# Performance work log

Measured on AMD Instinct MI355X. Metric: run time of the kernel, lower is better.

## Reference

```python
import jax, jax.numpy as jnp
import numpy as np

N_NODES = 50000
N_EDGES = 800000
IN_F = 512
H_F = 32
HEADS = 8
N_CLS = 40
NEG_SLOPE = 0.2


def gat_conv(h, W, al, ar, b, src, dst, n_heads, d_out):
    """DGL-style GATConv. h: [N, F_in]; W: [F_in, n_heads*d_out];
    al, ar: [n_heads, d_out]; b: [n_heads*d_out]. Returns [N, n_heads, d_out]."""
    n = h.shape[0]
    feat = (h @ W).reshape(n, n_heads, d_out)            # [N, H, D]
    el = jnp.sum(feat * al[None], axis=-1)               # [N, H]
    er = jnp.sum(feat * ar[None], axis=-1)               # [N, H]
    e = jax.nn.leaky_relu(el[src] + er[dst], NEG_SLOPE)  # [E, H]
    # numerically stable edge softmax per destination node
    m = jax.ops.segment_max(e, dst, num_segments=n)      # [N, H]
    m = jnp.where(jnp.isfinite(m), m, 0.0)
    ee = jnp.exp(e - m[dst])                             # [E, H]
    den = jax.ops.segment_sum(ee, dst, num_segments=n)   # [N, H]
    alpha = ee / jnp.maximum(den[dst], 1e-9)             # [E, H]
    msg = alpha[:, :, None] * feat[src]                  # [E, H, D]
    rst = jax.ops.segment_sum(msg, dst, num_segments=n)  # [N, H, D]
    return rst + b.reshape(1, n_heads, d_out)


def setup_inputs() -> dict:
    key = jax.random.key(0)
    ks = jax.random.split(key, 16)
    hid = H_F * HEADS
    s = lambda fan: 1.0 / np.sqrt(fan)
    return {
        "in_feat": jax.random.normal(ks[0], (N_NODES, IN_F), jnp.float32),
        "src": jax.random.randint(ks[1], (N_EDGES,), 0, N_NODES, jnp.int32),
        "dst": jax.random.randint(ks[2], (N_EDGES,), 0, N_NODES, jnp.int32),
        "W0": jax.random.normal(ks[3], (IN_F, hid), jnp.float32) * s(IN_F),
        "al0": jax.random.normal(ks[4], (HEADS, H_F), jnp.float32) * s(H_F),
        "ar0": jax.random.normal(ks[5], (HEADS, H_F), jnp.float32) * s(H_F),
        "b0": jnp.zeros((hid,), jnp.float32),
        "W1": jax.random.normal(ks[6], (hid, hid), jnp.float32) * s(hid),
        "al1": jax.random.normal(ks[7], (HEADS, H_F), jnp.float32) * s(H_F),
        "ar1": jax.random.normal(ks[8], (HEADS, H_F), jnp.float32) * s(H_F),
        "b1": jnp.zeros((hid,), jnp.float32),
        "W2": jax.random.normal(ks[9], (hid, N_CLS), jnp.float32) * s(hid),
        "al2": jax.random.normal(ks[10], (1, N_CLS), jnp.float32) * s(N_CLS),
        "ar2": jax.random.normal(ks[11], (1, N_CLS), jnp.float32) * s(N_CLS),
        "b2": jnp.zeros((N_CLS,), jnp.float32),
    }


def reference(in_feat, src, dst, W0, al0, ar0, b0, W1, al1, ar1, b1,
              W2, al2, ar2, b2):
    n = in_feat.shape[0]
    # layer 0 + ReLU (dropout p=0.0 is identity) + flatten heads
    h = gat_conv(in_feat, W0, al0, ar0, b0, src, dst, HEADS, H_F)
    h = jax.nn.relu(h).reshape(n, -1)
    # layer 1
    h = gat_conv(h, W1, al1, ar1, b1, src, dst, HEADS, H_F)
    h = jax.nn.relu(h).reshape(n, -1)
    # output layer, single head, no activation
    h = gat_conv(h, W2, al2, ar2, b2, src, dst, 1, N_CLS)
    return h.reshape(n, -1)
```

## Files before the change

### kernel.cpp

```cpp
#include <hip/hip_runtime.h>
#include <hip/hip_bf16.h>

#define N_NODES 50000
#define N_EDGES 800000
#define IN_F 512
#define HID 256
#define HEADS 8
#define DHEAD 32
#define N_CLS 40
#define NCLS_PAD 64

typedef __bf16 bf16x8 __attribute__((ext_vector_type(8)));
typedef float f32x4 __attribute__((ext_vector_type(4)));
typedef float f32x2 __attribute__((ext_vector_type(2)));

#define AT_AL0 0
#define AT_AR0 256
#define AT_AL1 512
#define AT_AR1 768
#define AT_AL2 1024
#define AT_AR2 1088
#define AT_B0  1152
#define AT_B1  1408
#define AT_B2  1664
#define AT_SZ  1792

__device__ __forceinline__ float ldflag(const void* p, long long i, int isbf) {
  return isbf ? __bfloat162float(((const __hip_bfloat16*)p)[i])
              : ((const float*)p)[i];
}
__device__ __forceinline__ float blo(unsigned u) { return __uint_as_float(u << 16); }
__device__ __forceinline__ float bhi(unsigned u) { return __uint_as_float(u & 0xffff0000u); }
__device__ __forceinline__ f32x2 bpair(unsigned u) {
  f32x2 r;
  r.x = __uint_as_float(u << 16);
  r.y = __uint_as_float(u & 0xffff0000u);
  return r;
}
__device__ __forceinline__ unsigned pk2(float a, float b) {
  unsigned x = __bfloat16_as_ushort(__float2bfloat16(a));
  unsigned y = __bfloat16_as_ushort(__float2bfloat16(b));
  return x | (y << 16);
}
__device__ __forceinline__ uint4 ldA8(const void* A, int isbf, size_t base) {
  if (isbf) return *(const uint4*)((const unsigned short*)A + base);
  const float* ap = (const float*)A + base;
  float4 f1 = *(const float4*)ap;
  float4 f2 = *(const float4*)(ap + 4);
  return make_uint4(pk2(f1.x, f1.y), pk2(f1.z, f1.w), pk2(f2.x, f2.y), pk2(f2.z, f2.w));
}
__device__ __forceinline__ bf16x8 as_bf(uint4 v) {
  union { uint4 u; bf16x8 b; } x; x.u = v; return x.b;
}

__global__ void k_detect_prep(const unsigned short* __restrict__ raw, int* __restrict__ flag,
                              const void* al0, const void* ar0, const void* al1, const void* ar1,
                              const void* al2, const void* ar2, const void* b0, const void* b1,
                              const void* b2, float* __restrict__ att, int* __restrict__ cursor) {
  __shared__ int cnt[256];
  int t = threadIdx.x;
  for (int i = t; i < N_NODES; i += 256) cursor[i] = 0;
  int c = 0;
  for (int i = t; i < 8192; i += 256) {
    int e = (raw[i] >> 7) & 0xFF;
    if (e >= 0x90) c++;
  }
  cnt[t] = c;
  __syncthreads();
  for (int s = 128; s; s >>= 1) {
    if (t < s) cnt[t] += cnt[t + s];
    __syncthreads();
  }
  __shared__ int sflag;
  if (t == 0) { sflag = (cnt[0] > 64) ? 0 : 1; *flag = sflag; }
  __syncthreads();
  int isbf = sflag;
  att[AT_AL0 + t] = ldflag(al0, t, isbf);
  att[AT_AR0 + t] = ldflag(ar0, t, isbf);
  att[AT_AL1 + t] = ldflag(al1, t, isbf);
  att[AT_AR1 + t] = ldflag(ar1, t, isbf);
  att[AT_B0 + t]  = ldflag(b0, t, isbf);
  att[AT_B1 + t]  = ldflag(b1, t, isbf);
  if (t < N_CLS) {
    att[AT_AL2 + t] = ldflag(al2, t, isbf);
    att[AT_AR2 + t] = ldflag(ar2, t, isbf);
    att[AT_B2 + t]  = ldflag(b2, t, isbf);
  }
}

__global__ void k_hist(const int* __restrict__ dst, int* __restrict__ cnt) {
  int e = blockIdx.x * blockDim.x + threadIdx.x;
  if (e < N_EDGES) atomicAdd(&cnt[dst[e]], 1);
}

#define SCAN_B 512
#define SCAN_NB ((N_NODES + SCAN_B - 1) / SCAN_B)

__global__ __launch_bounds__(SCAN_B) void k_scan_blocks(const int* __restrict__ deg,
                                                        int* __restrict__ excl,
                                                        int* __restrict__ partial) {
  __shared__ int buf[SCAN_B];
  int t = threadIdx.x;
  int i = blockIdx.x * SCAN_B + t;
  int v = (i < N_NODES) ? deg[i] : 0;
  buf[t] = v;
  __syncthreads();
  for (int off = 1; off < SCAN_B; off <<= 1) {
    int x = (t >= off) ? buf[t - off] : 0;
    __syncthreads();
    buf[t] += x;
    __syncthreads();
  }
  if (i < N_NODES) excl[i] = buf[t] - v;
  if (t == SCAN_B - 1) partial[blockIdx.x] = buf[t];
}

__global__ void k_scan_partials(int* __restrict__ partial, int* __restrict__ rowptr) {
  __shared__ int buf[SCAN_NB];
  int t = threadIdx.x;
  if (t < SCAN_NB) buf[t] = partial[t];
  __syncthreads();
  if (t == 0) {
    int run = 0;
    for (int b = 0; b < SCAN_NB; b++) { int v = buf[b]; buf[b] = run; run += v; }
    rowptr[N_NODES] = run;
  }
  __syncthreads();
  if (t < SCAN_NB) partial[t] = buf[t];
}

__global__ void k_scan_add(int* __restrict__ rowptr, const int* __restrict__ partial,
                           int* __restrict__ cursor) {
  int i = blockIdx.x * blockDim.x + threadIdx.x;
  if (i < N_NODES) {
    rowptr[i] += partial[i / SCAN_B];
    cursor[i] = 0;
  }
}

__global__ void k_scatter(const int* __restrict__ src, const int* __restrict__ dst,
                          const int* __restrict__ rowptr, int* __restrict__ cursor,
                          int* __restrict__ csr_src) {
  int e = blockIdx.x * blockDim.x + threadIdx.x;
  if (e < N_EDGES) {
    int d = dst[e];
    int pos = rowptr[d] + atomicAdd(&cursor[d], 1);
    csr_src[pos] = src[e];
  }
}

#define TW0 (HID * IN_F)
#define TW1 (TW0 + HID * HID)
#define TW2 (TW1 + NCLS_PAD * HID)
__global__ void k_transpose_all(const void* __restrict__ W0, const void* __restrict__ W1,
                                const void* __restrict__ W2,
                                __hip_bfloat16* __restrict__ w0t, __hip_bfloat16* __restrict__ w1t,
                                __hip_bfloat16* __restrict__ w2t, const int* __restrict__ flag) {
  int isbf = *flag;
  int i = blockIdx.x * blockDim.x + threadIdx.x;
  if (i < TW0) {
    int n = i >> 9, k = i & 511;
    w0t[i] = __float2bfloat16(ldflag(W0, (long long)k * HID + n, isbf));
  } else if (i < TW1) {
    int j = i - TW0;
    int n = j >> 8, k = j & 255;
    w1t[j] = __float2bfloat16(ldflag(W1, (long long)k * HID + n, isbf));
  } else if (i < TW2) {
    int j = i - TW1;
    int n = j >> 8, k = j & 255;
    float v = (n < N_CLS) ? ldflag(W2, (long long)k * N_CLS + n, isbf) : 0.f;
    w2t[j] = __float2bfloat16(v);
  }
}

__global__ __launch_bounds__(256) void k_gemmw(const void* __restrict__ A,
                                               const __hip_bfloat16* __restrict__ Bt,
                                               __hip_bfloat16* __restrict__ C,
                                               int M, int K, int N,
                                               const int* __restrict__ flag, int force_bf,
                                               const float* __restrict__ al,
                                               const float* __restrict__ ar,
                                               float* __restrict__ el,
                                               float* __restrict__ er, int fuse_eler) {
  const int isbf = force_bf ? 1 : *flag;
  int nblk = N >> 6;
  int wave = threadIdx.x >> 6, lane = threadIdx.x & 63;
  int tile = blockIdx.x * 4 + wave;
  int mb = tile / nblk;
  int nb = tile - mb * nblk;
  int m0 = mb * 64, n0 = nb * 64;
  if (m0 >= M) return;
  int lm = lane & 15, quad = lane >> 4;
  int koff = quad << 3;
  size_t ab[4];
  const unsigned short* bb[4];
  #pragma unroll
  for (int i = 0; i < 4; i++) {
    int ga = m0 + i * 16 + lm;
    if (ga > M - 1) ga = M - 1;
    ab[i] = (size_t)ga * K + koff;
    bb[i] = (const unsigned short*)Bt + (size_t)(n0 + i * 16 + lm) * K + koff;
  }
  f32x4 acc[4][4] = {};
  uint4 a0[4], b0[4];
  #pragma unroll
  for (int i = 0; i < 4; i++) { a0[i] = ldA8(A, isbf, ab[i]); b0[i] = *(const uint4*)bb[i]; }
  int nk = K >> 5;
  for (int t = 1; t < nk; ++t) {
    int k0 = t << 5;
    uint4 a1[4], b1[4];
    #pragma unroll
    for (int i = 0; i < 4; i++) {
      a1[i] = ldA8(A, isbf, ab[i] + k0);
      b1[i] = *(const uint4*)(bb[i] + k0);
    }
    #pragma unroll
    for (int mi = 0; mi < 4; mi++)
      #pragma unroll
      for (int ni = 0; ni < 4; ni++)
        acc[mi][ni] = __builtin_amdgcn_mfma_f32_16x16x32_bf16(as_bf(a0[mi]), as_bf(b0[ni]),
                                                              acc[mi][ni], 0, 0, 0);
    #pragma unroll
    for (int i = 0; i < 4; i++) { a0[i] = a1[i]; b0[i] = b1[i]; }
  }
  #pragma unroll
  for (int mi = 0; mi < 4; mi++)
    #pragma unroll
    for (int ni = 0; ni < 4; ni++)
      acc[mi][ni] = __builtin_amdgcn_mfma_f32_16x16x32_bf16(as_bf(a0[mi]), as_bf(b0[ni]),
                                                            acc[mi][ni], 0, 0, 0);
  #pragma unroll
  for (int mi = 0; mi < 4; mi++) {
    #pragma unroll
    for (int r2 = 0; r2 < 4; r2++) {
      int gm = m0 + mi * 16 + (quad << 2) + r2;
      if (gm < M) {
        #pragma unroll
        for (int ni = 0; ni < 4; ni++) {
          int gn = n0 + ni * 16 + lm;
          C[(size_t)gm * N + gn] = __float2bfloat16(acc[mi][ni][r2]);
        }
      }
    }
  }
  if (fuse_eler) {
    int h0 = n0 >> 5;
    float ala[4], ara[4];
    #pragma unroll
    for (int ni = 0; ni < 4; ni++) {
      int idx = (h0 + (ni >> 1)) * DHEAD + ((ni & 1) << 4) + lm;
      ala[ni] = al[idx];
      ara[ni] = ar[idx];
    }
    #pragma unroll
    for (int mi = 0; mi < 4; mi++)
      #pragma unroll
      for (int r2 = 0; r2 < 4; r2++) {
        int gm = m0 + mi * 16 + (quad << 2) + r2;
        #pragma unroll
        for (int hp = 0; hp < 2; hp++) {
          float pl = acc[mi][2 * hp][r2] * ala[2 * hp] + acc[mi][2 * hp + 1][r2] * ala[2 * hp + 1];
          float pr = acc[mi][2 * hp][r2] * ara[2 * hp] + acc[mi][2 * hp + 1][r2] * ara[2 * hp + 1];
          #pragma unroll
          for (int d = 1; d < 16; d <<= 1) {
            pl += __shfl_xor(pl, d, 16);
            pr += __shfl_xor(pr, d, 16);
          }
          if (lm == 0 && gm < M) {
            el[gm * HEADS + h0 + hp] = pl;
            er[gm * HEADS + h0 + hp] = pr;
          }
        }
      }
  }
}

__global__ void k_eler2(const __hip_bfloat16* __restrict__ feat2,
                        const float* __restrict__ al, const float* __restrict__ ar,
                        float* __restrict__ el, float* __restrict__ er) {
  int n = blockIdx.x * blockDim.x + threadIdx.x;
  if (n >= N_NODES) return;
  const __hip_bfloat16* f = feat2 + (size_t)n * NCLS_PAD;
  float sl = 0.f, sr = 0.f;
  for (int d = 0; d < N_CLS; d++) {
    float v = __bfloat162float(f[d]);
    sl += v * al[d];
    sr += v * ar[d];
  }
  el[n] = sl;
  er[n] = sr;
}

__global__ __launch_bounds__(256) void k_aggregate8(const int* __restrict__ rowptr,
                                                    const int* __restrict__ csr_src,
                                                    const uint4* __restrict__ feat_rows,
                                                    const float* __restrict__ el,
                                                    const float* __restrict__ er,
                                                    const float* __restrict__ bias,
                                                    __hip_bfloat16* __restrict__ out) {
  __shared__ float lds_acc[8][256];
  __shared__ float lds_l[8][32];
  int n = blockIdx.x;
  int t = threadIdx.x;
  int slot = t >> 5;
  int c = t & 31;
  int hh = c >> 2;
  float er_n = er[n * HEADS + hh];
  int beg = rowptr[n], end = rowptr[n + 1];
  float l = 0.f;
  f32x2 a0 = {0.f, 0.f}, a1 = {0.f, 0.f}, a2 = {0.f, 0.f}, a3 = {0.f, 0.f};
  const char* fb = (const char*)feat_rows;
  unsigned cb = (unsigned)c << 4;
  int i = beg + slot;
  for (; i + 8 < end; i += 16) {
    int s1 = csr_src[i];
    int s2 = csr_src[i + 8];
    float el1 = el[s1 * HEADS + hh];
    float el2 = el[s2 * HEADS + hh];
    uint4 f1 = *(const uint4*)(fb + (((unsigned)s1 << 9) | cb));
    uint4 f2 = *(const uint4*)(fb + (((unsigned)s2 << 9) | cb));
    float x1 = el1 + er_n, x2 = el2 + er_n;
    float e1 = x1 > 0.f ? x1 : 0.2f * x1;
    float e2 = x2 > 0.f ? x2 : 0.2f * x2;
    float p1 = __expf(fminf(e1, 60.f));
    float p2 = __expf(fminf(e2, 60.f));
    l += p1 + p2;
    a0 += bpair(f1.x) * p1; a1 += bpair(f1.y) * p1;
    a2 += bpair(f1.z) * p1; a3 += bpair(f1.w) * p1;
    a0 += bpair(f2.x) * p2; a1 += bpair(f2.y) * p2;
    a2 += bpair(f2.z) * p2; a3 += bpair(f2.w) * p2;
  }
  if (i < end) {
    int s = csr_src[i];
    float elv = el[s * HEADS + hh];
    uint4 fv = *(const uint4*)(fb + (((unsigned)s << 9) | cb));
    float x = elv + er_n;
    float e = x > 0.f ? x : 0.2f * x;
    float p = __expf(fminf(e, 60.f));
    l += p;
    a0 += bpair(fv.x) * p; a1 += bpair(fv.y) * p;
    a2 += bpair(fv.z) * p; a3 += bpair(fv.w) * p;
  }
  *(float4*)&lds_acc[slot][c * 8]     = make_float4(a0.x, a0.y, a1.x, a1.y);
  *(float4*)&lds_acc[slot][c * 8 + 4] = make_float4(a2.x, a2.y, a3.x, a3.y);
  lds_l[slot][c] = l;
  __syncthreads();
  float a = 0.f, L = 0.f;
  #pragma unroll
  for (int s2 = 0; s2 < 8; s2++) { a += lds_acc[s2][t]; L += lds_l[s2][t >> 3]; }
  float o = a / fmaxf(L, 1e-9f) + bias[t];
  o = fmaxf(o, 0.f);
  out[(size_t)n * HID + t] = __float2bfloat16(o);
}

__global__ __launch_bounds__(256) void k_aggregate1(const int* __restrict__ rowptr,
                                                    const int* __restrict__ csr_src,
                                                    const uint4* __restrict__ fr2,
                                                    const float* __restrict__ el,
                                                    const float* __restrict__ er,
                                                    const float* __restrict__ bias,
                                                    void* __restrict__ out,
                                                    const int* __restrict__ flag) {
  __shared__ float lds_acc[32][64];
  __shared__ float lds_l[32][8];
  int isbf = *flag;
  int n = blockIdx.x;
  int t = threadIdx.x;
  int slot = t >> 3;
  int c = t & 7;
  float er_n = er[n];
  int beg = rowptr[n], end = rowptr[n + 1];
  float l = 0.f;
  f32x2 a0 = {0.f, 0.f}, a1 = {0.f, 0.f}, a2 = {0.f, 0.f}, a3 = {0.f, 0.f};
  const char* fb = (const char*)fr2;
  unsigned cb = (unsigned)c << 4;
  int i = beg + slot;
  for (; i + 32 < end; i += 64) {
    int s1 = csr_src[i], s2 = csr_src[i + 32];
    float el1 = el[s1], el2 = el[s2];
    uint4 f1 = *(const uint4*)(fb + (((unsigned)s1 << 7) | cb));
    uint4 f2 = *(const uint4*)(fb + (((unsigned)s2 << 7) | cb));
    float x1 = el1 + er_n, x2 = el2 + er_n;
    float e1 = x1 > 0.f ? x1 : 0.2f * x1;
    float e2 = x2 > 0.f ? x2 : 0.2f * x2;
    float p1 = __expf(fminf(e1, 60.f));
    float p2 = __expf(fminf(e2, 60.f));
    l += p1 + p2;
    a0 += bpair(f1.x) * p1; a1 += bpair(f1.y) * p1;
    a2 += bpair(f1.z) * p1; a3 += bpair(f1.w) * p1;
    a0 += bpair(f2.x) * p2; a1 += bpair(f2.y) * p2;
    a2 += bpair(f2.z) * p2; a3 += bpair(f2.w) * p2;
  }
  if (i < end) {
    int s = csr_src[i];
    float x = el[s] + er_n;
    uint4 fv = *(const uint4*)(fb + (((unsigned)s << 7) | cb));
    float e = x > 0.f ? x : 0.2f * x;
    float p = __expf(fminf(e, 60.f));
    l += p;
    a0 += bpair(fv.x) * p; a1 += bpair(fv.y) * p;
    a2 += bpair(fv.z) * p; a3 += bpair(fv.w) * p;
  }
  *(float4*)&lds_acc[slot][c * 8]     = make_float4(a0.x, a0.y, a1.x, a1.y);
  *(float4*)&lds_acc[slot][c * 8 + 4] = make_float4(a2.x, a2.y, a3.x, a3.y);
  lds_l[slot][c] = l;
  __syncthreads();
  if (t < N_CLS) {
    float a = 0.f, L = 0.f;
    #pragma unroll
    for (int s2 = 0; s2 < 32; s2++) { a += lds_acc[s2][t]; L += lds_l[s2][t >> 3]; }
    float o = a / fmaxf(L, 1e-9f) + bias[t];
    if (isbf) ((__hip_bfloat16*)out)[(size_t)n * N_CLS + t] = __float2bfloat16(o);
    else      ((float*)out)[(size_t)n * N_CLS + t] = o;
  }
}

static inline size_t align_up(size_t x) { return (x + 255) & ~(size_t)255; }

extern "C" void kernel_launch(void* const* d_in, const int* in_sizes, int n_in,
                              void* d_out, int out_size, void* d_ws, size_t ws_size,
                              hipStream_t stream) {
  const void* in_feat = d_in[0];
  const int* src = (const int*)d_in[1];
  const int* dst = (const int*)d_in[2];
  const void* W0  = d_in[3];
  const void* al0 = d_in[4];
  const void* ar0 = d_in[5];
  const void* b0  = d_in[6];
  const void* W1  = d_in[7];
  const void* al1 = d_in[8];
  const void* ar1 = d_in[9];
  const void* b1  = d_in[10];
  const void* W2  = d_in[11];
  const void* al2 = d_in[12];
  const void* ar2 = d_in[13];
  const void* b2  = d_in[14];

  char* p = (char*)d_ws;
  int* flag = (int*)p;                   p += 256;
  float* att = (float*)p;                p += align_up(AT_SZ * sizeof(float));
  int* rowptr = (int*)p;                 p += align_up((N_NODES + 1) * sizeof(int));
  int* cursor = (int*)p;                 p += align_up(N_NODES * sizeof(int));
  int* csr_src = (int*)p;                p += align_up(N_EDGES * sizeof(int));
  int* partial = (int*)p;                p += align_up(SCAN_NB * sizeof(int));
  __hip_bfloat16* feat16 = (__hip_bfloat16*)p; p += align_up((size_t)N_NODES * HID * sizeof(__hip_bfloat16));
  __hip_bfloat16* h16 = (__hip_bfloat16*)p;    p += align_up((size_t)N_NODES * HID * sizeof(__hip_bfloat16));
  float* el = (float*)p;                 p += align_up((size_t)N_NODES * HEADS * sizeof(float));
  float* er = (float*)p;                 p += align_up((size_t)N_NODES * HEADS * sizeof(float));
  __hip_bfloat16* w0t = (__hip_bfloat16*)p;    p += align_up((size_t)HID * IN_F * sizeof(__hip_bfloat16));
  __hip_bfloat16* w1t = (__hip_bfloat16*)p;    p += align_up((size_t)HID * HID * sizeof(__hip_bfloat16));
  __hip_bfloat16* w2t = (__hip_bfloat16*)p;    p += align_up((size_t)NCLS_PAD * HID * sizeof(__hip_bfloat16));

  const int EB = (N_EDGES + 255) / 256;
  const int MB64 = (N_NODES + 63) / 64;
  const int GW01 = MB64;
  const int GW2 = (MB64 + 3) / 4;

  k_detect_prep<<<1, 256, 0, stream>>>((const unsigned short*)in_feat, flag,
                                       al0, ar0, al1, ar1, al2, ar2, b0, b1, b2, att, cursor);

  k_hist<<<EB, 256, 0, stream>>>(dst, cursor);
  k_scan_blocks<<<SCAN_NB, SCAN_B, 0, stream>>>(cursor, rowptr, partial);
  k_scan_partials<<<1, 128, 0, stream>>>(partial, rowptr);
  k_scan_add<<<(N_NODES + 255) / 256, 256, 0, stream>>>(rowptr, partial, cursor);
  k_scatter<<<EB, 256, 0, stream>>>(src, dst, rowptr, cursor, csr_src);

  k_transpose_all<<<(TW2 + 255) / 256, 256, 0, stream>>>(W0, W1, W2, w0t, w1t, w2t, flag);

  k_gemmw<<<GW01, 256, 0, stream>>>(in_feat, w0t, feat16, N_NODES, IN_F, HID, flag, 0,
                                    att + AT_AL0, att + AT_AR0, el, er, 1);
  k_aggregate8<<<N_NODES, 256, 0, stream>>>(rowptr, csr_src, (const uint4*)feat16, el, er, att + AT_B0, h16);

  k_gemmw<<<GW01, 256, 0, stream>>>(h16, w1t, feat16, N_NODES, HID, HID, flag, 1,
                                    att + AT_AL1, att + AT_AR1, el, er, 1);
  k_aggregate8<<<N_NODES, 256, 0, stream>>>(rowptr, csr_src, (const uint4*)feat16, el, er, att + AT_B1, h16);

  k_gemmw<<<GW2, 256, 0, stream>>>(h16, w2t, feat16, N_NODES, HID, NCLS_PAD, flag, 1,
                                   nullptr, nullptr, nullptr, nullptr, 0);
  k_eler2<<<(N_NODES + 255) / 256, 256, 0, stream>>>(feat16, att + AT_AL2, att + AT_AR2, el, er);
  k_aggregate1<<<N_NODES, 256, 0, stream>>>(rowptr, csr_src, (const uint4*)feat16, el, er, att + AT_B2, d_out, flag);
}
```

Baseline: 625.4 us.

## Shrink GEMM wave tiles to 32x32 with XCD-aware block remap and deeper prefetch

Each wave of the feature-transform GEMM now computes a 32x32 output tile instead of 64x64, so four times as many tiles are launched and fewer registers are used per wave. Block indices are remapped so that consecutive logical tiles land on the same XCD, which is meant to improve L2 reuse of the shared A rows. Global loads are prefetched two k-steps ahead instead of one to hide latency. The cost is less data reuse per wave, since each A and B fragment now feeds fewer MFMAs, which raises total global and L2 traffic.

```diff
diff --git a/kernel.cpp b/kernel.cpp
--- a/kernel.cpp
+++ b/kernel.cpp
@@ -173,103 +173,101 @@
   }
 }
 
-__global__ __launch_bounds__(256) void k_gemmw(const void* __restrict__ A,
-                                               const __hip_bfloat16* __restrict__ Bt,
-                                               __hip_bfloat16* __restrict__ C,
-                                               int M, int K, int N,
-                                               const int* __restrict__ flag, int force_bf,
-                                               const float* __restrict__ al,
-                                               const float* __restrict__ ar,
-                                               float* __restrict__ el,
-                                               float* __restrict__ er, int fuse_eler) {
+__global__ __launch_bounds__(256) void k_gemmw32(const void* __restrict__ A,
+                                                 const __hip_bfloat16* __restrict__ Bt,
+                                                 __hip_bfloat16* __restrict__ C,
+                                                 int M, int K, int N,
+                                                 const int* __restrict__ flag, int force_bf,
+                                                 const float* __restrict__ al,
+                                                 const float* __restrict__ ar,
+                                                 float* __restrict__ el,
+                                                 float* __restrict__ er, int fuse_eler) {
   const int isbf = force_bf ? 1 : *flag;
-  int nblk = N >> 6;
+  int nblk = N >> 5;
+  int mb32 = (M + 31) >> 5;
+  int ntiles = mb32 * nblk;
+  int nwg = gridDim.x;
+  int q = nwg >> 3, r = nwg & 7;
+  int xcd = blockIdx.x & 7, lid = blockIdx.x >> 3;
+  int logical = (xcd < r ? xcd * (q + 1) : r * (q + 1) + (xcd - r) * q) + lid;
   int wave = threadIdx.x >> 6, lane = threadIdx.x & 63;
-  int tile = blockIdx.x * 4 + wave;
+  int tile = logical * 4 + wave;
+  if (tile >= ntiles) return;
   int mb = tile / nblk;
   int nb = tile - mb * nblk;
-  int m0 = mb * 64, n0 = nb * 64;
-  if (m0 >= M) return;
+  int m0 = mb << 5, n0 = nb << 5;
   int lm = lane & 15, quad = lane >> 4;
   int koff = quad << 3;
-  size_t ab[4];
-  const unsigned short* bb[4];
+  size_t ab0, ab1;
+  {
+    int ga0 = m0 + lm;      if (ga0 > M - 1) ga0 = M - 1;
+    int ga1 = m0 + 16 + lm; if (ga1 > M - 1) ga1 = M - 1;
+    ab0 = (size_t)ga0 * K + koff;
+    ab1 = (size_t)ga1 * K + koff;
+  }
+  const unsigned short* bb0 = (const unsigned short*)Bt + (size_t)(n0 + lm) * K + koff;
+  const unsigned short* bb1 = (const unsigned short*)Bt + (size_t)(n0 + 16 + lm) * K + koff;
+  f32x4 acc[2][2] = {};
+  int nk = K >> 5;
+  uint4 aS0_0, aS0_1, bS0_0, bS0_1;
+  uint4 aS1_0, aS1_1, bS1_0, bS1_1;
+  aS0_0 = ldA8(A, isbf, ab0);       aS0_1 = ldA8(A, isbf, ab1);
+  bS0_0 = *(const uint4*)bb0;       bS0_1 = *(const uint4*)bb1;
+  if (nk > 1) {
+    aS1_0 = ldA8(A, isbf, ab0 + 32);  aS1_1 = ldA8(A, isbf, ab1 + 32);
+    bS1_0 = *(const uint4*)(bb0 + 32); bS1_1 = *(const uint4*)(bb1 + 32);
+  }
+  for (int t = 0; t < nk; ++t) {
+    uint4 aS2_0, aS2_1, bS2_0, bS2_1;
+    bool pre = (t + 2) < nk;
+    if (pre) {
+      int k2 = (t + 2) << 5;
+      aS2_0 = ldA8(A, isbf, ab0 + k2);  aS2_1 = ldA8(A, isbf, ab1 + k2);
+      bS2_0 = *(const uint4*)(bb0 + k2); bS2_1 = *(const uint4*)(bb1 + k2);
+    }
+    acc[0][0] = __builtin_amdgcn_mfma_f32_16x16x32_bf16(as_bf(aS0_0), as_bf(bS0_0), acc[0][0], 0, 0, 0);
+    acc[0][1] = __builtin_amdgcn_mfma_f32_16x16x32_bf16(as_bf(aS0_0), as_bf(bS0_1), acc[0][1], 0, 0, 0);
+    acc[1][0] = __builtin_amdgcn_mfma_f32_16x16x32_bf16(as_bf(aS0_1), as_bf(bS0_0), acc[1][0], 0, 0, 0);
+    acc[1][1] = __builtin_amdgcn_mfma_f32_16x16x32_bf16(as_bf(aS0_1), as_bf(bS0_1), acc[1][1], 0, 0, 0);
+    aS0_0 = aS1_0; aS0_1 = aS1_1; bS0_0 = bS1_0; bS0_1 = bS1_1;
+    if (pre) { aS1_0 = aS2_0; aS1_1 = aS2_1; bS1_0 = bS2_0; bS1_1 = bS2_1; }
+  }
   #pragma unroll
-  for (int i = 0; i < 4; i++) {
-    int ga = m0 + i * 16 + lm;
-    if (ga > M - 1) ga = M - 1;
-    ab[i] = (size_t)ga * K + koff;
-    bb[i] = (const unsigned short*)Bt + (size_t)(n0 + i * 16 + lm) * K + koff;
-  }
-  f32x4 acc[4][4] = {};
-  uint4 a0[4], b0[4];
-  #pragma unroll
-  for (int i = 0; i < 4; i++) { a0[i] = ldA8(A, isbf, ab[i]); b0[i] = *(const uint4*)bb[i]; }
-  int nk = K >> 5;
-  for (int t = 1; t < nk; ++t) {
-    int k0 = t << 5;
-    uint4 a1[4], b1[4];
-    #pragma unroll
-    for (int i = 0; i < 4; i++) {
-      a1[i] = ldA8(A, isbf, ab[i] + k0);
-      b1[i] = *(const uint4*)(bb[i] + k0);
-    }
-    #pragma unroll
-    for (int mi = 0; mi < 4; mi++)
-      #pragma unroll
-      for (int ni = 0; ni < 4; ni++)
-        acc[mi][ni] = __builtin_amdgcn_mfma_f32_16x16x32_bf16(as_bf(a0[mi]), as_bf(b0[ni]),
-                                                              acc[mi][ni], 0, 0, 0);
-    #pragma unroll
-    for (int i = 0; i < 4; i++) { a0[i] = a1[i]; b0[i] = b1[i]; }
-  }
-  #pragma unroll
-  for (int mi = 0; mi < 4; mi++)
-    #pragma unroll
-    for (int ni = 0; ni < 4; ni++)
-      acc[mi][ni] = __builtin_amdgcn_mfma_f32_16x16x32_bf16(as_bf(a0[mi]), as_bf(b0[ni]),
-                                                            acc[mi][ni], 0, 0, 0);
-  #pragma unroll
-  for (int mi = 0; mi < 4; mi++) {
+  for (int mi = 0; mi < 2; mi++)
     #pragma unroll
     for (int r2 = 0; r2 < 4; r2++) {
       int gm = m0 + mi * 16 + (quad << 2) + r2;
       if (gm < M) {
         #pragma unroll
-        for (int ni = 0; ni < 4; ni++) {
+        for (int ni = 0; ni < 2; ni++) {
           int gn = n0 + ni * 16 + lm;
           C[(size_t)gm * N + gn] = __float2bfloat16(acc[mi][ni][r2]);
         }
       }
     }
-  }
   if (fuse_eler) {
-    int h0 = n0 >> 5;
-    float ala[4], ara[4];
+    int hg = n0 >> 5;
+    float ala[2], ara[2];
     #pragma unroll
-    for (int ni = 0; ni < 4; ni++) {
-      int idx = (h0 + (ni >> 1)) * DHEAD + ((ni & 1) << 4) + lm;
-      ala[ni] = al[idx];
-      ara[ni] = ar[idx];
+    for (int ni = 0; ni < 2; ni++) {
+      ala[ni] = al[hg * DHEAD + ni * 16 + lm];
+      ara[ni] = ar[hg * DHEAD + ni * 16 + lm];
     }
     #pragma unroll
-    for (int mi = 0; mi < 4; mi++)
+    for (int mi = 0; mi < 2; mi++)
       #pragma unroll
       for (int r2 = 0; r2 < 4; r2++) {
+        float pl = acc[mi][0][r2] * ala[0] + acc[mi][1][r2] * ala[1];
+        float pr = acc[mi][0][r2] * ara[0] + acc[mi][1][r2] * ara[1];
+        #pragma unroll
+        for (int d = 1; d < 16; d <<= 1) {
+          pl += __shfl_xor(pl, d, 16);
+          pr += __shfl_xor(pr, d, 16);
+        }
         int gm = m0 + mi * 16 + (quad << 2) + r2;
-        #pragma unroll
-        for (int hp = 0; hp < 2; hp++) {
-          float pl = acc[mi][2 * hp][r2] * ala[2 * hp] + acc[mi][2 * hp + 1][r2] * ala[2 * hp + 1];
-          float pr = acc[mi][2 * hp][r2] * ara[2 * hp] + acc[mi][2 * hp + 1][r2] * ara[2 * hp + 1];
-          #pragma unroll
-          for (int d = 1; d < 16; d <<= 1) {
-            pl += __shfl_xor(pl, d, 16);
-            pr += __shfl_xor(pr, d, 16);
-          }
-          if (lm == 0 && gm < M) {
-            el[gm * HEADS + h0 + hp] = pl;
-            er[gm * HEADS + h0 + hp] = pr;
-          }
+        if (lm == 0 && gm < M) {
+          el[gm * HEADS + hg] = pl;
+          er[gm * HEADS + hg] = pr;
         }
       }
   }
@@ -452,9 +450,9 @@
   __hip_bfloat16* w2t = (__hip_bfloat16*)p;    p += align_up((size_t)NCLS_PAD * HID * sizeof(__hip_bfloat16));
 
   const int EB = (N_EDGES + 255) / 256;
-  const int MB64 = (N_NODES + 63) / 64;
-  const int GW01 = MB64;
-  const int GW2 = (MB64 + 3) / 4;
+  const int MB32 = (N_NODES + 31) / 32;
+  const int GW01 = (MB32 * 8 + 3) / 4;
+  const int GW2  = (MB32 * 2 + 3) / 4;
 
   k_detect_prep<<<1, 256, 0, stream>>>((const unsigned short*)in_feat, flag,
                                        al0, ar0, al1, ar1, al2, ar2, b0, b1, b2, att, cursor);
@@ -467,16 +465,16 @@
 
   k_transpose_all<<<(TW2 + 255) / 256, 256, 0, stream>>>(W0, W1, W2, w0t, w1t, w2t, flag);
 
-  k_gemmw<<<GW01, 256, 0, stream>>>(in_feat, w0t, feat16, N_NODES, IN_F, HID, flag, 0,
-                                    att + AT_AL0, att + AT_AR0, el, er, 1);
+  k_gemmw32<<<GW01, 256, 0, stream>>>(in_feat, w0t, feat16, N_NODES, IN_F, HID, flag, 0,
+                                      att + AT_AL0, att + AT_AR0, el, er, 1);
   k_aggregate8<<<N_NODES, 256, 0, stream>>>(rowptr, csr_src, (const uint4*)feat16, el, er, att + AT_B0, h16);
 
-  k_gemmw<<<GW01, 256, 0, stream>>>(h16, w1t, feat16, N_NODES, HID, HID, flag, 1,
-                                    att + AT_AL1, att + AT_AR1, el, er, 1);
+  k_gemmw32<<<GW01, 256, 0, stream>>>(h16, w1t, feat16, N_NODES, HID, HID, flag, 1,
+                                      att + AT_AL1, att + AT_AR1, el, er, 1);
   k_aggregate8<<<N_NODES, 256, 0, stream>>>(rowptr, csr_src, (const uint4*)feat16, el, er, att + AT_B1, h16);
 
-  k_gemmw<<<GW2, 256, 0, stream>>>(h16, w2t, feat16, N_NODES, HID, NCLS_PAD, flag, 1,
-                                   nullptr, nullptr, nullptr, nullptr, 0);
+  k_gemmw32<<<GW2, 256, 0, stream>>>(h16, w2t, feat16, N_NODES, HID, NCLS_PAD, flag, 1,
+                                     nullptr, nullptr, nullptr, nullptr, 0);
   k_eler2<<<(N_NODES + 255) / 256, 256, 0, stream>>>(feat16, att + AT_AL2, att + AT_AR2, el, er);
   k_aggregate1<<<N_NODES, 256, 0, stream>>>(rowptr, csr_src, (const uint4*)feat16, el, er, att + AT_B2, d_out, flag);
 }
```

Result: slower. 673.9 us (+7.8%).
